# Kernel tuning notes

Hardware: AMD Instinct MI355X
Metric: run time of the kernel (lower is better)

Reference implementation:

```python
import jax, jax.numpy as jnp
import numpy as np

N, D_IN, D_OUT = 262144, 80, 160
EPS = 1e-5


def setup_inputs() -> dict:
    key = jax.random.key(0)
    ks = jax.random.split(key, 9)
    s = 1.0 / np.sqrt(D_IN)
    return {
        "sub": jax.random.normal(ks[0], (N, D_IN), jnp.float32),
        "left": jax.random.normal(ks[1], (N, D_IN), jnp.float32),
        "right": jax.random.normal(ks[2], (N, D_IN), jnp.float32),
        "W_sub": jax.random.normal(ks[3], (D_OUT, D_IN), jnp.float32) * s,
        "b_sub": jax.random.normal(ks[4], (D_OUT,), jnp.float32) * s,
        "g_sub": jnp.ones((D_OUT,), jnp.float32),
        "be_sub": jnp.zeros((D_OUT,), jnp.float32),
        "W_left": jax.random.normal(ks[5], (D_OUT, D_IN), jnp.float32) * s,
        "b_left": jax.random.normal(ks[6], (D_OUT,), jnp.float32) * s,
        "g_left": jnp.ones((D_OUT,), jnp.float32),
        "be_left": jnp.zeros((D_OUT,), jnp.float32),
        "W_right": jax.random.normal(ks[7], (D_OUT, D_IN), jnp.float32) * s,
        "b_right": jax.random.normal(ks[8], (D_OUT,), jnp.float32) * s,
        "g_right": jnp.ones((D_OUT,), jnp.float32),
        "be_right": jnp.zeros((D_OUT,), jnp.float32),
    }


def _lin_bn(x, W, b, gamma, beta):
    # Linear + BatchNorm1d (training mode: batch mean, biased var, eps=1e-5)
    h = x @ W.T + b                      # [N, 160]
    mu = jnp.mean(h, axis=0)
    var = jnp.mean(jnp.square(h - mu), axis=0)
    return (h - mu) * jax.lax.rsqrt(var + EPS) * gamma + beta


def reference(sub, left, right,
              W_sub, b_sub, g_sub, be_sub,
              W_left, b_left, g_left, be_left,
              W_right, b_right, g_right, be_right):
    R_sub = _lin_bn(sub, W_sub, b_sub, g_sub, be_sub)
    R_left = _lin_bn(left, W_left, b_left, g_left, be_left)
    R_right = _lin_bn(right, W_right, b_right, g_right, be_right)
    # diag(A @ B.T) == rowwise dot product — same math, O(N*D)
    sub_left = jnp.sum(R_sub * R_left, axis=1)    # [N]
    sub_right = jnp.sum(R_sub * R_right, axis=1)  # [N]
    left_right = jnp.sum(R_left * R_right, axis=1)  # [N]
    all_sim = jnp.stack([sub_left, sub_right, left_right], axis=0)  # [3, N]
    p = jax.nn.softmax(all_sim, axis=0)           # [3, N]
    x_storke = (p[0][:, None] * left
                + p[1][:, None] * right
                + p[2][:, None] * sub)            # [N, 80]
    return x_storke
```

## Files before the change

kernel.cpp:

```cpp
#include <hip/hip_runtime.h>

#define N_ROWS 262144
#define D 80
#define DA 81
#define MSTRIDE 84
#define DOUT 160
#define EPS 1e-5f

#define S_OFF   0
#define S_SIZE  (DA * DA)
#define T_OFF   (3 * S_SIZE)
#define T_SIZE  (DOUT * DA)
#define WP_OFF  (T_OFF + 3 * T_SIZE)
#define WP_SIZE (DOUT * DA)
#define MC_OFF  ((WP_OFF + 3 * WP_SIZE + 3) & ~3)
#define MC_SIZE (DA * MSTRIDE)
#define AUG_OFF (MC_OFF + 3 * MC_SIZE)
#define AUG_SIZE 84

#define K1_BLOCKS 512
#define K1_ROWS   (N_ROWS / K1_BLOCKS)
#define K1_NT     (K1_ROWS / 32)

__global__ __launch_bounds__(256) void k1_moments(const float* __restrict__ xs,
                                                  const float* __restrict__ xl,
                                                  const float* __restrict__ xr,
                                                  float* __restrict__ ws) {
    const float* x = (blockIdx.y == 0) ? xs : (blockIdx.y == 1) ? xl : xr;
    float* S = ws + S_OFF + blockIdx.y * S_SIZE;

    __shared__ float lds[2 * 2560 + 3600];

    const int tid = threadIdx.x;
    const int wave = tid >> 6;
    const int lane = tid & 63;

    int ti = -1, tj = -1;
    if (lane < 55) {
        int l = lane, a = 0;
        while (l >= 10 - a) { l -= 10 - a; a++; }
        ti = a; tj = a + l;
    }

    float acc[8][8];
#pragma unroll
    for (int u = 0; u < 8; u++)
#pragma unroll
        for (int v = 0; v < 8; v++) acc[u][v] = 0.f;
    float csum[8];
#pragma unroll
    for (int u = 0; u < 8; u++) csum[u] = 0.f;

    const size_t base = (size_t)blockIdx.x * K1_ROWS * D;
    const float4* __restrict__ gsrc = reinterpret_cast<const float4*>(x + base);

    float4 r0, r1, r2;
    r0 = gsrc[tid]; r1 = gsrc[tid + 256]; if (tid < 128) r2 = gsrc[tid + 512];
    {
        float4* d4 = reinterpret_cast<float4*>(lds);
        d4[tid] = r0; d4[tid + 256] = r1; if (tid < 128) d4[tid + 512] = r2;
    }

    for (int t = 0; t < K1_NT; t++) {
        __syncthreads();
        if (t + 1 < K1_NT) {
            const float4* __restrict__ s = gsrc + (size_t)(t + 1) * 640;
            r0 = s[tid]; r1 = s[tid + 256]; if (tid < 128) r2 = s[tid + 512];
        }
        const float* __restrict__ buf = lds + (t & 1) * 2560;
        if (ti >= 0) {
            const int rbase = wave * 8;
#pragma unroll 2
            for (int rr = 0; rr < 8; rr++) {
                const float* row = &buf[(rbase + rr) * D];
                float a8[8], b8[8];
                *reinterpret_cast<float4*>(&a8[0]) = *reinterpret_cast<const float4*>(&row[ti * 8]);
                *reinterpret_cast<float4*>(&a8[4]) = *reinterpret_cast<const float4*>(&row[ti * 8 + 4]);
                *reinterpret_cast<float4*>(&b8[0]) = *reinterpret_cast<const float4*>(&row[tj * 8]);
                *reinterpret_cast<float4*>(&b8[4]) = *reinterpret_cast<const float4*>(&row[tj * 8 + 4]);
#pragma unroll
                for (int u = 0; u < 8; u++)
#pragma unroll
                    for (int v = 0; v < 8; v++) acc[u][v] += a8[u] * b8[v];
                if (ti == tj) {
#pragma unroll
                    for (int u = 0; u < 8; u++) csum[u] += a8[u];
                }
            }
        }
        if (t + 1 < K1_NT) {
            float4* d4 = reinterpret_cast<float4*>(lds + ((t + 1) & 1) * 2560);
            d4[tid] = r0; d4[tid + 256] = r1; if (tid < 128) d4[tid + 512] = r2;
        }
    }

    float* red = lds + 5120;
    __syncthreads();
    for (int i = tid; i < 3600; i += 256) red[i] = 0.f;
    __syncthreads();
    for (int w = 0; w < 4; w++) {
        if (wave == w && ti >= 0) {
            float* dst = &red[lane * 64];
#pragma unroll
            for (int u = 0; u < 8; u++)
#pragma unroll
                for (int v = 0; v < 8; v++) dst[u * 8 + v] += acc[u][v];
            if (ti == tj) {
#pragma unroll
                for (int u = 0; u < 8; u++) red[3520 + ti * 8 + u] += csum[u];
            }
        }
        __syncthreads();
    }

    for (int e = tid; e < 3520; e += 256) {
        int p = e >> 6, o = e & 63;
        int l = p, a = 0;
        while (l >= 10 - a) { l -= 10 - a; a++; }
        const int pi = a, pj = a + l;
        const int i = pi * 8 + (o >> 3), j = pj * 8 + (o & 7);
        const float v = red[e];
        atomicAdd(&S[i * DA + j], v);
        if (pi != pj) atomicAdd(&S[j * DA + i], v);
    }
    for (int c = tid; c < D; c += 256) {
        const float v = red[3520 + c];
        atomicAdd(&S[c * DA + D], v);
        atomicAdd(&S[D * DA + c], v);
    }
}

__global__ void k2_T(const float* __restrict__ Ws, const float* __restrict__ bs,
                     const float* __restrict__ Wl, const float* __restrict__ bl,
                     const float* __restrict__ Wr, const float* __restrict__ br,
                     float* __restrict__ ws) {
    int e = blockIdx.x * 256 + threadIdx.x;
    if (e >= 3 * DOUT * DA) return;
    int p = e / (DOUT * DA);
    int rem = e - p * (DOUT * DA);
    int j = rem / DA, i = rem - j * DA;

    const float* W = (p == 0) ? Ws : (p == 1) ? Wl : Wr;
    const float* b = (p == 0) ? bs : (p == 1) ? bl : br;
    const float* S = ws + S_OFF + p * S_SIZE;

    float a0 = 0.f, a1 = 0.f;
    for (int k = 0; k < D; k += 2) {
        a0 += W[j * D + k] * S[k * DA + i];
        a1 += W[j * D + k + 1] * S[(k + 1) * DA + i];
    }
    float s80 = (i == D) ? (float)N_ROWS : S[D * DA + i];
    ws[T_OFF + p * T_SIZE + j * DA + i] = a0 + a1 + b[j] * s80;
}

__global__ void k2_scale(const float* __restrict__ Ws, const float* __restrict__ bs,
                         const float* __restrict__ gs, const float* __restrict__ bes,
                         const float* __restrict__ Wl, const float* __restrict__ bl,
                         const float* __restrict__ gl, const float* __restrict__ bel,
                         const float* __restrict__ Wr, const float* __restrict__ br,
                         const float* __restrict__ gr, const float* __restrict__ ber,
                         float* __restrict__ ws) {
    int e = blockIdx.x * 256 + threadIdx.x;
    if (e >= 3 * DOUT) return;
    int p = e / DOUT, j = e - p * DOUT;

    const float* W  = (p == 0) ? Ws  : (p == 1) ? Wl  : Wr;
    const float* b  = (p == 0) ? bs  : (p == 1) ? bl  : br;
    const float* g  = (p == 0) ? gs  : (p == 1) ? gl  : gr;
    const float* be = (p == 0) ? bes : (p == 1) ? bel : ber;

    const float* T = ws + T_OFF + p * T_SIZE + j * DA;
    float eh2 = 0.f;
    for (int k = 0; k < D; k++) eh2 += T[k] * W[j * D + k];
    eh2 += T[D] * b[j];
    const float invN = 1.0f / (float)N_ROWS;
    eh2 *= invN;
    float mu = T[D] * invN;
    float var = eh2 - mu * mu;
    float a = g[j] * rsqrtf(var + EPS);

    float* Wp = ws + WP_OFF + p * WP_SIZE + j * DA;
    for (int k = 0; k < D; k++) Wp[k] = a * W[j * D + k];
    Wp[D] = a * b[j] + be[j] - a * mu;
}

__global__ void k2_M(float* __restrict__ ws) {
    int e = blockIdx.x * 256 + threadIdx.x;
    if (e >= 3 * DA * DA) return;
    int q = e / (DA * DA);
    int rem = e - q * (DA * DA);
    int k = rem / DA, i = rem - k * DA;

    int pa = (q == 2) ? 1 : 0;
    int pb = (q == 0) ? 1 : 2;
    const float* Wa = ws + WP_OFF + pa * WP_SIZE;
    const float* Wb = ws + WP_OFF + pb * WP_SIZE;

    float a0 = 0.f, a1 = 0.f;
    for (int j = 0; j < DOUT; j += 2) {
        a0 += Wa[j * DA + i] * Wb[j * DA + k];
        a1 += Wa[(j + 1) * DA + i] * Wb[(j + 1) * DA + k];
    }
    float v = a0 + a1;
    ws[MC_OFF + q * MC_SIZE + k * MSTRIDE + i] = v;
    if (i == D) ws[AUG_OFF + q * AUG_SIZE + k] = v;
}

#define G_IG   20
#define G_RG   16
#define G_RT   4
#define G_ROWS (G_RG * G_RT)
#define G_TPB  (G_IG * G_RG)
#define XLD    84

__device__ __forceinline__ void gemm_partial(const float* __restrict__ Mc,
                                             const float* __restrict__ Xk,
                                             const float* __restrict__ dotb,
                                             int dotStride,
                                             int ig, int rg,
                                             float* __restrict__ sred) {
    const int i0 = ig * 4;
    float z[G_RT][4];
#pragma unroll
    for (int r = 0; r < G_RT; r++) { z[r][0] = z[r][1] = z[r][2] = z[r][3] = 0.f; }

#pragma unroll 2
    for (int kb = 0; kb < 20; kb++) {
        float4 m[4];
#pragma unroll
        for (int j = 0; j < 4; j++)
            m[j] = *reinterpret_cast<const float4*>(&Mc[(kb * 4 + j) * MSTRIDE + i0]);
#pragma unroll
        for (int r = 0; r < G_RT; r++) {
            float4 xk = *reinterpret_cast<const float4*>(&Xk[(rg * G_RT + r) * XLD + kb * 4]);
            z[r][0] += m[0].x * xk.x; z[r][1] += m[0].y * xk.x; z[r][2] += m[0].z * xk.x; z[r][3] += m[0].w * xk.x;
            z[r][0] += m[1].x * xk.y; z[r][1] += m[1].y * xk.y; z[r][2] += m[1].z * xk.y; z[r][3] += m[1].w * xk.y;
            z[r][0] += m[2].x * xk.z; z[r][1] += m[2].y * xk.z; z[r][2] += m[2].z * xk.z; z[r][3] += m[2].w * xk.z;
            z[r][0] += m[3].x * xk.w; z[r][1] += m[3].y * xk.w; z[r][2] += m[3].z * xk.w; z[r][3] += m[3].w * xk.w;
        }
    }
    {
        float4 m80 = *reinterpret_cast<const float4*>(&Mc[D * MSTRIDE + i0]);
#pragma unroll
        for (int r = 0; r < G_RT; r++) {
            z[r][0] += m80.x; z[r][1] += m80.y; z[r][2] += m80.z; z[r][3] += m80.w;
        }
    }
#pragma unroll
    for (int r = 0; r < G_RT; r++) {
        const int row = rg * G_RT + r;
        float4 w4 = *reinterpret_cast<const float4*>(&dotb[(size_t)row * dotStride + i0]);
        sred[row * 21 + ig] = z[r][0] * w4.x + z[r][1] * w4.y + z[r][2] * w4.z + z[r][3] * w4.w;
    }
}

__global__ __launch_bounds__(G_TPB, 4) void k3_main(const float* __restrict__ xs_g,
                                                    const float* __restrict__ xl_g,
                                                    const float* __restrict__ xr_g,
                                                    const float* __restrict__ ws,
                                                    float* __restrict__ out) {
    __shared__ float Xl[G_ROWS * XLD];
    __shared__ float Xr[G_ROWS * XLD];
    __shared__ float sred[G_ROWS * 21];
    __shared__ float parr[G_ROWS * 4];
    __shared__ float augl[3 * AUG_SIZE];

    const int tid = threadIdx.x;
    const int ig = tid % G_IG;
    const int rg = tid / G_IG;
    const size_t rowBase = (size_t)blockIdx.x * G_ROWS;

    const float* Mc0 = ws + MC_OFF + 0 * MC_SIZE;
    const float* Mc1 = ws + MC_OFF + 1 * MC_SIZE;
    const float* Mc2 = ws + MC_OFF + 2 * MC_SIZE;
    const float* subb = xs_g + rowBase * D;

    {
        const float4* gl = reinterpret_cast<const float4*>(xl_g + rowBase * D);
        const float4* gr = reinterpret_cast<const float4*>(xr_g + rowBase * D);
#pragma unroll
        for (int it = 0; it < 4; it++) {
            int u = tid + it * G_TPB;
            int r = u / 20, c = u % 20;
            *reinterpret_cast<float4*>(&Xl[r * XLD + c * 4]) = gl[u];
            *reinterpret_cast<float4*>(&Xr[r * XLD + c * 4]) = gr[u];
        }
        if (tid < 3 * AUG_SIZE) augl[tid] = ws[AUG_OFF + tid];
    }
    __syncthreads();

    float s0r = 0.f, s1r = 0.f, s2r = 0.f;

    gemm_partial(Mc0, Xl, subb, D, ig, rg, sred);
    __syncthreads();
    if (tid < G_ROWS) {
        float a = 0.f;
#pragma unroll
        for (int c = 0; c < 20; c++) a += sred[tid * 21 + c];
        float b = augl[0 * AUG_SIZE + D];
#pragma unroll
        for (int c = 0; c < 20; c++) {
            float4 u4 = *reinterpret_cast<const float4*>(&augl[0 * AUG_SIZE + c * 4]);
            float4 x4 = *reinterpret_cast<const float4*>(&Xl[tid * XLD + c * 4]);
            b += u4.x * x4.x + u4.y * x4.y + u4.z * x4.z + u4.w * x4.w;
        }
        s0r = a + b;
    }
    __syncthreads();

    gemm_partial(Mc1, Xr, subb, D, ig, rg, sred);
    __syncthreads();
    if (tid < G_ROWS) {
        float a = 0.f;
#pragma unroll
        for (int c = 0; c < 20; c++) a += sred[tid * 21 + c];
        float b = augl[1 * AUG_SIZE + D];
#pragma unroll
        for (int c = 0; c < 20; c++) {
            float4 u4 = *reinterpret_cast<const float4*>(&augl[1 * AUG_SIZE + c * 4]);
            float4 x4 = *reinterpret_cast<const float4*>(&Xr[tid * XLD + c * 4]);
            b += u4.x * x4.x + u4.y * x4.y + u4.z * x4.z + u4.w * x4.w;
        }
        s1r = a + b;
    }
    __syncthreads();

    gemm_partial(Mc2, Xr, Xl, XLD, ig, rg, sred);
    __syncthreads();
    if (tid < G_ROWS) {
        float a = 0.f;
#pragma unroll
        for (int c = 0; c < 20; c++) a += sred[tid * 21 + c];
        float b = augl[2 * AUG_SIZE + D];
#pragma unroll
        for (int c = 0; c < 20; c++) {
            float4 u4 = *reinterpret_cast<const float4*>(&augl[2 * AUG_SIZE + c * 4]);
            float4 x4 = *reinterpret_cast<const float4*>(&Xr[tid * XLD + c * 4]);
            b += u4.x * x4.x + u4.y * x4.y + u4.z * x4.z + u4.w * x4.w;
        }
        s2r = a + b;

        float m = fmaxf(s0r, fmaxf(s1r, s2r));
        float e0 = __expf(s0r - m), e1 = __expf(s1r - m), e2 = __expf(s2r - m);
        float inv = 1.0f / (e0 + e1 + e2);
        parr[tid * 4 + 0] = e0 * inv;
        parr[tid * 4 + 1] = e1 * inv;
        parr[tid * 4 + 2] = e2 * inv;
    }
    __syncthreads();

    {
        const float4* gs = reinterpret_cast<const float4*>(subb);
        float4* go = reinterpret_cast<float4*>(out + rowBase * D);
#pragma unroll
        for (int it = 0; it < 4; it++) {
            int u = tid + it * G_TPB;
            int r = u / 20, c = u % 20;
            float p0 = parr[r * 4 + 0], p1 = parr[r * 4 + 1], p2 = parr[r * 4 + 2];
            float4 L = *reinterpret_cast<const float4*>(&Xl[r * XLD + c * 4]);
            float4 R = *reinterpret_cast<const float4*>(&Xr[r * XLD + c * 4]);
            float4 S = gs[u];
            float4 o;
            o.x = p0 * L.x + p1 * R.x + p2 * S.x;
            o.y = p0 * L.y + p1 * R.y + p2 * S.y;
            o.z = p0 * L.z + p1 * R.z + p2 * S.z;
            o.w = p0 * L.w + p1 * R.w + p2 * S.w;
            go[u] = o;
        }
    }
}

extern "C" void kernel_launch(void* const* d_in, const int* in_sizes, int n_in,
                              void* d_out, int out_size, void* d_ws, size_t ws_size,
                              hipStream_t stream) {
    const float* xs = (const float*)d_in[0];
    const float* xl = (const float*)d_in[1];
    const float* xr = (const float*)d_in[2];
    const float* Wsub = (const float*)d_in[3];
    const float* bsub = (const float*)d_in[4];
    const float* gsub = (const float*)d_in[5];
    const float* besub = (const float*)d_in[6];
    const float* Wleft = (const float*)d_in[7];
    const float* bleft = (const float*)d_in[8];
    const float* gleft = (const float*)d_in[9];
    const float* beleft = (const float*)d_in[10];
    const float* Wright = (const float*)d_in[11];
    const float* bright = (const float*)d_in[12];
    const float* gright = (const float*)d_in[13];
    const float* beright = (const float*)d_in[14];
    float* ws = (float*)d_ws;
    float* out = (float*)d_out;

    hipMemsetAsync(ws + S_OFF, 0, 3 * S_SIZE * sizeof(float), stream);

    k1_moments<<<dim3(K1_BLOCKS, 3), 256, 0, stream>>>(xs, xl, xr, ws);
    k2_T<<<(3 * DOUT * DA + 255) / 256, 256, 0, stream>>>(
        Wsub, bsub, Wleft, bleft, Wright, bright, ws);
    k2_scale<<<(3 * DOUT + 255) / 256, 256, 0, stream>>>(
        Wsub, bsub, gsub, besub, Wleft, bleft, gleft, beleft,
        Wright, bright, gright, beright, ws);
    k2_M<<<(3 * DA * DA + 255) / 256, 256, 0, stream>>>(ws);
    k3_main<<<N_ROWS / G_ROWS, G_TPB, 0, stream>>>(xs, xl, xr, ws, out);
}
```

Measured before the change: 699.0 us.

## Share one LDS tile across passes, fuse aug dot, raise occupancy in main kernel

The main kernel now holds a single shared-memory X tile instead of separate left and right tiles. The left tile is reloaded from global memory for the final output, and the augmented-vector dot product is folded into each gemm pass, so the serial per-row reduction loops go away. The two gemm passes that use the right tile run back to back with two reduction buffers, which drops a barrier, and launch bounds go from 4 to 5 blocks per CU. The moment kernel now writes only the upper triangle of S with half the atomics, and the T kernel reads S symmetrically. The trade-off is extra global reads of the left input, which should be served from L2.

```diff
diff --git a/kernel.cpp b/kernel.cpp
--- a/kernel.cpp
+++ b/kernel.cpp
@@ -119,14 +119,10 @@
         while (l >= 10 - a) { l -= 10 - a; a++; }
         const int pi = a, pj = a + l;
         const int i = pi * 8 + (o >> 3), j = pj * 8 + (o & 7);
-        const float v = red[e];
-        atomicAdd(&S[i * DA + j], v);
-        if (pi != pj) atomicAdd(&S[j * DA + i], v);
+        atomicAdd(&S[i * DA + j], red[e]);
     }
     for (int c = tid; c < D; c += 256) {
-        const float v = red[3520 + c];
-        atomicAdd(&S[c * DA + D], v);
-        atomicAdd(&S[D * DA + c], v);
+        atomicAdd(&S[c * DA + D], red[3520 + c]);
     }
 }
 
@@ -144,13 +140,14 @@
     const float* b = (p == 0) ? bs : (p == 1) ? bl : br;
     const float* S = ws + S_OFF + p * S_SIZE;
 
-    float a0 = 0.f, a1 = 0.f;
-    for (int k = 0; k < D; k += 2) {
+    float a0 = 0.f;
+    const int kmid = (i < D) ? (i + 1) : D;
+    for (int k = 0; k < kmid; k++)
         a0 += W[j * D + k] * S[k * DA + i];
-        a1 += W[j * D + k + 1] * S[(k + 1) * DA + i];
-    }
-    float s80 = (i == D) ? (float)N_ROWS : S[D * DA + i];
-    ws[T_OFF + p * T_SIZE + j * DA + i] = a0 + a1 + b[j] * s80;
+    for (int k = kmid; k < D; k++)
+        a0 += W[j * D + k] * S[i * DA + k];
+    float s80 = (i == D) ? (float)N_ROWS : S[i * DA + D];
+    ws[T_OFF + p * T_SIZE + j * DA + i] = a0 + b[j] * s80;
 }
 
 __global__ void k2_scale(const float* __restrict__ Ws, const float* __restrict__ bs,
@@ -212,13 +209,14 @@
 #define G_ROWS (G_RG * G_RT)
 #define G_TPB  (G_IG * G_RG)
 #define XLD    84
-
-__device__ __forceinline__ void gemm_partial(const float* __restrict__ Mc,
-                                             const float* __restrict__ Xk,
-                                             const float* __restrict__ dotb,
-                                             int dotStride,
-                                             int ig, int rg,
-                                             float* __restrict__ sred) {
+#define SRED_LD 20
+
+__device__ __forceinline__ void gemm_pass(const float* __restrict__ Mc,
+                                          const float* __restrict__ augq,
+                                          const float* __restrict__ X,
+                                          const float4* __restrict__ dot4,
+                                          int ig, int rg,
+                                          float* __restrict__ sred) {
     const int i0 = ig * 4;
     float z[G_RT][4];
 #pragma unroll
@@ -226,17 +224,17 @@
 
 #pragma unroll 2
     for (int kb = 0; kb < 20; kb++) {
-        float4 m[4];
-#pragma unroll
-        for (int j = 0; j < 4; j++)
-            m[j] = *reinterpret_cast<const float4*>(&Mc[(kb * 4 + j) * MSTRIDE + i0]);
+        float4 m0 = *reinterpret_cast<const float4*>(&Mc[(kb * 4 + 0) * MSTRIDE + i0]);
+        float4 m1 = *reinterpret_cast<const float4*>(&Mc[(kb * 4 + 1) * MSTRIDE + i0]);
+        float4 m2 = *reinterpret_cast<const float4*>(&Mc[(kb * 4 + 2) * MSTRIDE + i0]);
+        float4 m3 = *reinterpret_cast<const float4*>(&Mc[(kb * 4 + 3) * MSTRIDE + i0]);
 #pragma unroll
         for (int r = 0; r < G_RT; r++) {
-            float4 xk = *reinterpret_cast<const float4*>(&Xk[(rg * G_RT + r) * XLD + kb * 4]);
-            z[r][0] += m[0].x * xk.x; z[r][1] += m[0].y * xk.x; z[r][2] += m[0].z * xk.x; z[r][3] += m[0].w * xk.x;
-            z[r][0] += m[1].x * xk.y; z[r][1] += m[1].y * xk.y; z[r][2] += m[1].z * xk.y; z[r][3] += m[1].w * xk.y;
-            z[r][0] += m[2].x * xk.z; z[r][1] += m[2].y * xk.z; z[r][2] += m[2].z * xk.z; z[r][3] += m[2].w * xk.z;
-            z[r][0] += m[3].x * xk.w; z[r][1] += m[3].y * xk.w; z[r][2] += m[3].z * xk.w; z[r][3] += m[3].w * xk.w;
+            float4 xk = *reinterpret_cast<const float4*>(&X[(rg * G_RT + r) * XLD + kb * 4]);
+            z[r][0] += m0.x * xk.x; z[r][1] += m0.y * xk.x; z[r][2] += m0.z * xk.x; z[r][3] += m0.w * xk.x;
+            z[r][0] += m1.x * xk.y; z[r][1] += m1.y * xk.y; z[r][2] += m1.z * xk.y; z[r][3] += m1.w * xk.y;
+            z[r][0] += m2.x * xk.z; z[r][1] += m2.y * xk.z; z[r][2] += m2.z * xk.z; z[r][3] += m2.w * xk.z;
+            z[r][0] += m3.x * xk.w; z[r][1] += m3.y * xk.w; z[r][2] += m3.z * xk.w; z[r][3] += m3.w * xk.w;
         }
     }
     {
@@ -246,24 +244,27 @@
             z[r][0] += m80.x; z[r][1] += m80.y; z[r][2] += m80.z; z[r][3] += m80.w;
         }
     }
+    float4 av = *reinterpret_cast<const float4*>(&augq[i0]);
 #pragma unroll
     for (int r = 0; r < G_RT; r++) {
         const int row = rg * G_RT + r;
-        float4 w4 = *reinterpret_cast<const float4*>(&dotb[(size_t)row * dotStride + i0]);
-        sred[row * 21 + ig] = z[r][0] * w4.x + z[r][1] * w4.y + z[r][2] * w4.z + z[r][3] * w4.w;
-    }
-}
-
-__global__ __launch_bounds__(G_TPB, 4) void k3_main(const float* __restrict__ xs_g,
+        float4 xa = *reinterpret_cast<const float4*>(&X[row * XLD + i0]);
+        float4 w4 = dot4[row * 20 + ig];
+        sred[row * SRED_LD + ig] =
+            z[r][0] * w4.x + z[r][1] * w4.y + z[r][2] * w4.z + z[r][3] * w4.w
+            + av.x * xa.x + av.y * xa.y + av.z * xa.z + av.w * xa.w;
+    }
+}
+
+__global__ __launch_bounds__(G_TPB, 5) void k3_main(const float* __restrict__ xs_g,
                                                     const float* __restrict__ xl_g,
                                                     const float* __restrict__ xr_g,
                                                     const float* __restrict__ ws,
                                                     float* __restrict__ out) {
-    __shared__ float Xl[G_ROWS * XLD];
-    __shared__ float Xr[G_ROWS * XLD];
-    __shared__ float sred[G_ROWS * 21];
-    __shared__ float parr[G_ROWS * 4];
-    __shared__ float augl[3 * AUG_SIZE];
+    __shared__ __align__(16) float X[G_ROWS * XLD];
+    __shared__ __align__(16) float sredA[G_ROWS * SRED_LD];
+    __shared__ __align__(16) float sredB[G_ROWS * SRED_LD];
+    __shared__ __align__(16) float parr[G_ROWS * 4];
 
     const int tid = threadIdx.x;
     const int ig = tid % G_IG;
@@ -273,73 +274,54 @@
     const float* Mc0 = ws + MC_OFF + 0 * MC_SIZE;
     const float* Mc1 = ws + MC_OFF + 1 * MC_SIZE;
     const float* Mc2 = ws + MC_OFF + 2 * MC_SIZE;
-    const float* subb = xs_g + rowBase * D;
-
-    {
-        const float4* gl = reinterpret_cast<const float4*>(xl_g + rowBase * D);
-        const float4* gr = reinterpret_cast<const float4*>(xr_g + rowBase * D);
-#pragma unroll
-        for (int it = 0; it < 4; it++) {
-            int u = tid + it * G_TPB;
-            int r = u / 20, c = u % 20;
-            *reinterpret_cast<float4*>(&Xl[r * XLD + c * 4]) = gl[u];
-            *reinterpret_cast<float4*>(&Xr[r * XLD + c * 4]) = gr[u];
-        }
-        if (tid < 3 * AUG_SIZE) augl[tid] = ws[AUG_OFF + tid];
-    }
-    __syncthreads();
-
-    float s0r = 0.f, s1r = 0.f, s2r = 0.f;
-
-    gemm_partial(Mc0, Xl, subb, D, ig, rg, sred);
-    __syncthreads();
+    const float* aug0 = ws + AUG_OFF + 0 * AUG_SIZE;
+    const float* aug1 = ws + AUG_OFF + 1 * AUG_SIZE;
+    const float* aug2 = ws + AUG_OFF + 2 * AUG_SIZE;
+
+    const float4* gl = reinterpret_cast<const float4*>(xl_g + rowBase * D);
+    const float4* gr = reinterpret_cast<const float4*>(xr_g + rowBase * D);
+    const float4* gs = reinterpret_cast<const float4*>(xs_g + rowBase * D);
+
+    float s0r = 0.f, s1r, s2r;
+
+#pragma unroll
+    for (int it = 0; it < 4; it++) {
+        int u = tid + it * G_TPB;
+        int r = u / 20, c = u % 20;
+        *reinterpret_cast<float4*>(&X[r * XLD + c * 4]) = gl[u];
+    }
+    __syncthreads();
+
+    gemm_pass(Mc0, aug0, X, gs, ig, rg, sredA);
+    __syncthreads();
+
     if (tid < G_ROWS) {
-        float a = 0.f;
-#pragma unroll
-        for (int c = 0; c < 20; c++) a += sred[tid * 21 + c];
-        float b = augl[0 * AUG_SIZE + D];
-#pragma unroll
-        for (int c = 0; c < 20; c++) {
-            float4 u4 = *reinterpret_cast<const float4*>(&augl[0 * AUG_SIZE + c * 4]);
-            float4 x4 = *reinterpret_cast<const float4*>(&Xl[tid * XLD + c * 4]);
-            b += u4.x * x4.x + u4.y * x4.y + u4.z * x4.z + u4.w * x4.w;
-        }
-        s0r = a + b;
-    }
-    __syncthreads();
-
-    gemm_partial(Mc1, Xr, subb, D, ig, rg, sred);
-    __syncthreads();
+        float a = aug0[D];
+#pragma unroll
+        for (int c = 0; c < SRED_LD; c++) a += sredA[tid * SRED_LD + c];
+        s0r = a;
+    }
+#pragma unroll
+    for (int it = 0; it < 4; it++) {
+        int u = tid + it * G_TPB;
+        int r = u / 20, c = u % 20;
+        *reinterpret_cast<float4*>(&X[r * XLD + c * 4]) = gr[u];
+    }
+    __syncthreads();
+
+    gemm_pass(Mc1, aug1, X, gs, ig, rg, sredA);
+    gemm_pass(Mc2, aug2, X, gl, ig, rg, sredB);
+    __syncthreads();
+
     if (tid < G_ROWS) {
-        float a = 0.f;
-#pragma unroll
-        for (int c = 0; c < 20; c++) a += sred[tid * 21 + c];
-        float b = augl[1 * AUG_SIZE + D];
-#pragma unroll
-        for (int c = 0; c < 20; c++) {
-            float4 u4 = *reinterpret_cast<const float4*>(&augl[1 * AUG_SIZE + c * 4]);
-            float4 x4 = *reinterpret_cast<const float4*>(&Xr[tid * XLD + c * 4]);
-            b += u4.x * x4.x + u4.y * x4.y + u4.z * x4.z + u4.w * x4.w;
-        }
-        s1r = a + b;
-    }
-    __syncthreads();
-
-    gemm_partial(Mc2, Xr, Xl, XLD, ig, rg, sred);
-    __syncthreads();
-    if (tid < G_ROWS) {
-        float a = 0.f;
-#pragma unroll
-        for (int c = 0; c < 20; c++) a += sred[tid * 21 + c];
-        float b = augl[2 * AUG_SIZE + D];
-#pragma unroll
-        for (int c = 0; c < 20; c++) {
-            float4 u4 = *reinterpret_cast<const float4*>(&augl[2 * AUG_SIZE + c * 4]);
-            float4 x4 = *reinterpret_cast<const float4*>(&Xr[tid * XLD + c * 4]);
-            b += u4.x * x4.x + u4.y * x4.y + u4.z * x4.z + u4.w * x4.w;
-        }
-        s2r = a + b;
-
+        float a = aug1[D];
+        float b = aug2[D];
+#pragma unroll
+        for (int c = 0; c < SRED_LD; c++) {
+            a += sredA[tid * SRED_LD + c];
+            b += sredB[tid * SRED_LD + c];
+        }
+        s1r = a; s2r = b;
         float m = fmaxf(s0r, fmaxf(s1r, s2r));
         float e0 = __expf(s0r - m), e1 = __expf(s1r - m), e2 = __expf(s2r - m);
         float inv = 1.0f / (e0 + e1 + e2);
@@ -350,15 +332,14 @@
     __syncthreads();
 
     {
-        const float4* gs = reinterpret_cast<const float4*>(subb);
         float4* go = reinterpret_cast<float4*>(out + rowBase * D);
 #pragma unroll
         for (int it = 0; it < 4; it++) {
             int u = tid + it * G_TPB;
             int r = u / 20, c = u % 20;
             float p0 = parr[r * 4 + 0], p1 = parr[r * 4 + 1], p2 = parr[r * 4 + 2];
-            float4 L = *reinterpret_cast<const float4*>(&Xl[r * XLD + c * 4]);
-            float4 R = *reinterpret_cast<const float4*>(&Xr[r * XLD + c * 4]);
+            float4 L = gl[u];
+            float4 R = *reinterpret_cast<const float4*>(&X[r * XLD + c * 4]);
             float4 S = gs[u];
             float4 o;
             o.x = p0 * L.x + p1 * R.x + p2 * S.x;
```

New measurement: 670.9 us. 1.04x faster.
